# Performance work log

Hardware: AMD Instinct MI355X
Metric: run time of the kernel (lower is better)

The kernel has to match this reference:

```python
import jax, jax.numpy as jnp
import numpy as np

B, S, D = 8, 2048, 512
H, DK, DV = 8, 64, 64


def setup_inputs() -> dict:
    key = jax.random.key(0)
    ks = jax.random.split(key, 12)
    def xavier(k, shape):
        fan_in, fan_out = shape[0], shape[1]
        std = (2.0 / (fan_in + fan_out)) ** 0.5
        return jax.random.normal(k, shape, dtype=jnp.float32) * std
    return {
        "Q": jax.random.normal(ks[0], (B, S, D), dtype=jnp.float32),
        "K": jax.random.normal(ks[1], (B, S, D), dtype=jnp.float32),
        "V": jax.random.normal(ks[2], (B, S, D), dtype=jnp.float32),
        "W_q": xavier(ks[3], (D, H * DK)),
        "W_k": xavier(ks[4], (D, H * DK)),
        "W_v": xavier(ks[5], (D, H * DV)),
        "W_o": xavier(ks[6], (H * DV, D)),
        "W1": xavier(ks[7], (D, D)),  # linear1.weight, stored [out, in]
        "b1": jnp.zeros((D,), dtype=jnp.float32),
        "W2": xavier(ks[8], (D, D)),  # linear2.weight
        "b2": jnp.zeros((D,), dtype=jnp.float32),
    }


def reference(Q, K, V, W_q, W_k, W_v, W_o, W1, b1, W2, b2):
    eps = 1e-6
    bsz, q_len, _ = Q.shape
    # project and split heads: [B, S, H, dk]
    Qh = (Q @ W_q).reshape(bsz, q_len, H, DK)
    Kh = (K @ W_k).reshape(bsz, q_len, H, DK)
    Vh = (V @ W_v).reshape(bsz, q_len, H, DV)
    temperature = DK ** 0.5
    # scores: [B, H, Sq, Sk] (full O(N^2) matrix, as in original)
    scores = jnp.einsum('bqhd,bkhd->bhqk', Qh, Kh) / (temperature + eps)
    probs = jax.nn.softmax(scores, axis=-1)  # dropout = identity (eval)
    V_att = jnp.einsum('bhqk,bkhd->bqhd', probs, Vh).reshape(bsz, q_len, H * DV)
    attn_out = V_att @ W_o  # dropout = identity
    X = Q + attn_out
    # FFN: linear2(relu(linear1(X))); torch Linear: x @ W.T + b
    ffn = jax.nn.relu(X @ W1.T + b1) @ W2.T + b2
    return ffn + X
```

## Files before the change

### kernel.cpp

```cpp
#include <hip/hip_runtime.h>
#include <stdint.h>

typedef __bf16 bf16;
typedef bf16 bf16x8 __attribute__((ext_vector_type(8)));
typedef bf16 bf16x4 __attribute__((ext_vector_type(4)));
typedef float f32x2 __attribute__((ext_vector_type(2)));
typedef float f32x4 __attribute__((ext_vector_type(4)));
typedef float f32x16 __attribute__((ext_vector_type(16)));

#define AS1 __attribute__((address_space(1)))
#define AS3 __attribute__((address_space(3)))

__device__ __forceinline__ void gll16(const void* g, void* l) {
    __builtin_amdgcn_global_load_lds((const AS1 unsigned int*)g,
                                     (AS3 unsigned int*)l, 16, 0, 0);
}

__device__ __forceinline__ bf16 f2bf(float x) { return (bf16)x; }

__device__ __forceinline__ float fexp2(float x) { return __builtin_amdgcn_exp2f(x); }

#define QSCALE_LOG2E 0.18033685757f

__global__ void k_castw(const float* __restrict__ Wq, const float* __restrict__ Wk,
                        const float* __restrict__ Wv, const float* __restrict__ Wo,
                        const float* __restrict__ W1, const float* __restrict__ W2,
                        bf16* __restrict__ oq, bf16* __restrict__ ok, bf16* __restrict__ ov,
                        bf16* __restrict__ oo, bf16* __restrict__ o1, bf16* __restrict__ o2)
{
    const int z = blockIdx.y;
    const int idx = blockIdx.x * 256 + threadIdx.x;
    const float* src = z == 0 ? Wq : z == 1 ? Wk : z == 2 ? Wv : z == 3 ? Wo : z == 4 ? W1 : W2;
    bf16* dst = z == 0 ? oq : z == 1 ? ok : z == 2 ? ov : z == 3 ? oo : z == 4 ? o1 : o2;
    if (z < 4) {
        const int n = idx >> 9, k = idx & 511;
        dst[idx] = f2bf(src[(k << 9) + n]);
    } else {
        dst[idx] = f2bf(src[idx]);
    }
}

__device__ __forceinline__ void gemm_core(const bf16* __restrict__ A,
                                          const bf16* __restrict__ Bt,
                                          const int K, bf16* As, bf16* Bs,
                                          const int bm, const int bn,
                                          f32x4 acc[4][4])
{
    const int tid  = threadIdx.x;
    const int lane = tid & 63;
    const int wave = tid >> 6;
    const int g    = lane >> 4;
    const int l15  = lane & 15;
    const int wm   = (wave >> 1) * 64;
    const int wn   = (wave & 1) * 64;

    const int srow = tid >> 2;
    const int sk   = (tid & 3) * 8;
    const size_t aoff0 = (size_t)(bm + srow) * K + sk;
    const size_t aoff1 = (size_t)(bm + 64 + srow) * K + sk;
    const size_t boff0 = (size_t)(bn + srow) * K + sk;
    const size_t boff1 = (size_t)(bn + 64 + srow) * K + sk;
    char* asb = (char*)As + wave * 1024;
    char* bsb = (char*)Bs + wave * 1024;

    for (int kt = 0; kt < K; kt += 32) {
        __syncthreads();
        gll16(A + aoff0 + kt, asb);
        gll16(A + aoff1 + kt, asb + 4096);
        gll16(Bt + boff0 + kt, bsb);
        gll16(Bt + boff1 + kt, bsb + 4096);
        __syncthreads();
        bf16x8 af[4], bfv[4];
#pragma unroll
        for (int mi = 0; mi < 4; ++mi)
            af[mi] = *(const bf16x8*)&As[(wm + mi * 16 + l15) * 32 + g * 8];
#pragma unroll
        for (int ni = 0; ni < 4; ++ni)
            bfv[ni] = *(const bf16x8*)&Bs[(wn + ni * 16 + l15) * 32 + g * 8];
#pragma unroll
        for (int mi = 0; mi < 4; ++mi)
#pragma unroll
            for (int ni = 0; ni < 4; ++ni)
                acc[mi][ni] = __builtin_amdgcn_mfma_f32_16x16x32_bf16(
                    af[mi], bfv[ni], acc[mi][ni], 0, 0, 0);
    }
}

__device__ __forceinline__ void gemm_core_f32(const float* __restrict__ A,
                                              const bf16* __restrict__ Bt,
                                              const int K, bf16* As, bf16* Bs,
                                              const int bm, const int bn,
                                              f32x4 acc[4][4])
{
    const int tid  = threadIdx.x;
    const int lane = tid & 63;
    const int wave = tid >> 6;
    const int g    = lane >> 4;
    const int l15  = lane & 15;
    const int wm   = (wave >> 1) * 64;
    const int wn   = (wave & 1) * 64;

    const int srow = tid >> 2;
    const int sk   = (tid & 3) * 8;
    const size_t aoff0 = (size_t)(bm + srow) * K + sk;
    const size_t aoff1 = (size_t)(bm + 64 + srow) * K + sk;
    const size_t boff0 = (size_t)(bn + srow) * K + sk;
    const size_t boff1 = (size_t)(bn + 64 + srow) * K + sk;
    char* bsb = (char*)Bs + wave * 1024;
    char* adst = (char*)As + tid * 16;

    for (int kt = 0; kt < K; kt += 32) {
        __syncthreads();
        gll16(Bt + boff0 + kt, bsb);
        gll16(Bt + boff1 + kt, bsb + 4096);
        {
            float4 a0 = *(const float4*)(A + aoff0 + kt);
            float4 a1 = *(const float4*)(A + aoff0 + kt + 4);
            float4 a2 = *(const float4*)(A + aoff1 + kt);
            float4 a3 = *(const float4*)(A + aoff1 + kt + 4);
            bf16x8 c0, c1;
            c0[0] = f2bf(a0.x); c0[1] = f2bf(a0.y); c0[2] = f2bf(a0.z); c0[3] = f2bf(a0.w);
            c0[4] = f2bf(a1.x); c0[5] = f2bf(a1.y); c0[6] = f2bf(a1.z); c0[7] = f2bf(a1.w);
            c1[0] = f2bf(a2.x); c1[1] = f2bf(a2.y); c1[2] = f2bf(a2.z); c1[3] = f2bf(a2.w);
            c1[4] = f2bf(a3.x); c1[5] = f2bf(a3.y); c1[6] = f2bf(a3.z); c1[7] = f2bf(a3.w);
            *(bf16x8*)adst = c0;
            *(bf16x8*)(adst + 4096) = c1;
        }
        __syncthreads();
        bf16x8 af[4], bfv[4];
#pragma unroll
        for (int mi = 0; mi < 4; ++mi)
            af[mi] = *(const bf16x8*)&As[(wm + mi * 16 + l15) * 32 + g * 8];
#pragma unroll
        for (int ni = 0; ni < 4; ++ni)
            bfv[ni] = *(const bf16x8*)&Bs[(wn + ni * 16 + l15) * 32 + g * 8];
#pragma unroll
        for (int mi = 0; mi < 4; ++mi)
#pragma unroll
            for (int ni = 0; ni < 4; ++ni)
                acc[mi][ni] = __builtin_amdgcn_mfma_f32_16x16x32_bf16(
                    af[mi], bfv[ni], acc[mi][ni], 0, 0, 0);
    }
}

template<int EPI>
__global__ __launch_bounds__(256)
void k_gemm(const bf16* __restrict__ A, const bf16* __restrict__ Bt,
            const float* __restrict__ bias, const float* __restrict__ residf,
            const bf16* __restrict__ residb,
            float* __restrict__ Cf, bf16* __restrict__ Cb,
            int M, int N, int K)
{
    __shared__ bf16 As[128 * 32];
    __shared__ bf16 Bs[128 * 32];
    const int bm = blockIdx.y * 128, bn = blockIdx.x * 128;
    f32x4 acc[4][4] = {};
    gemm_core(A, Bt, K, As, Bs, bm, bn, acc);

    const int tid  = threadIdx.x;
    const int lane = tid & 63;
    const int wave = tid >> 6;
    const int g    = lane >> 4;
    const int l15  = lane & 15;
    const int wm   = (wave >> 1) * 64;
    const int wn   = (wave & 1) * 64;
    const int col0 = bn + wn + l15;
#pragma unroll
    for (int ni = 0; ni < 4; ++ni) {
        const int col = col0 + ni * 16;
        float bv = 0.f;
        if constexpr (EPI == 2 || EPI == 3) bv = bias[col];
#pragma unroll
        for (int mi = 0; mi < 4; ++mi) {
#pragma unroll
            for (int r = 0; r < 4; ++r) {
                const int row = bm + wm + mi * 16 + 4 * g + r;
                const size_t idx = (size_t)row * N + col;
                float v = acc[mi][ni][r];
                if constexpr (EPI == 1) {
                    Cb[idx] = f2bf(v + residf[idx]);
                } else if constexpr (EPI == 2) {
                    Cb[idx] = f2bf(fmaxf(v + bv, 0.f));
                } else {
                    Cf[idx] = v + bv + (float)residb[idx];
                }
            }
        }
    }
}

__global__ __launch_bounds__(256)
void k_proj(const float* __restrict__ Qf, const float* __restrict__ Kf, const float* __restrict__ Vf,
            const bf16* __restrict__ BQ, const bf16* __restrict__ BK, const bf16* __restrict__ BV,
            bf16* __restrict__ OQ, bf16* __restrict__ OK_, bf16* __restrict__ OV)
{
    __shared__ bf16 SM[8192];
    const int z = blockIdx.z;
    const float* A = z == 0 ? Qf : z == 1 ? Kf : Vf;
    const bf16* Bt = z == 0 ? BQ : z == 1 ? BK : BV;
    bf16* Cb       = z == 0 ? OQ : z == 1 ? OK_ : OV;
    const int bm = blockIdx.y * 128, bn = blockIdx.x * 128;
    f32x4 acc[4][4] = {};
    gemm_core_f32(A, Bt, 512, SM, SM + 4096, bm, bn, acc);

    const int tid  = threadIdx.x;
    const int lane = tid & 63;
    const int wave = tid >> 6;
    const int g    = lane >> 4;
    const int l15  = lane & 15;
    const int wn   = (wave & 1) * 64;
    const int bb   = bm >> 11;
    const int s0   = bm & 2047;

    __syncthreads();
#pragma unroll
    for (int p = 0; p < 2; ++p) {
        if ((wave >> 1) == p) {
            if (z == 0) {
#pragma unroll
                for (int ni = 0; ni < 4; ++ni) {
                    const int col = wn + ni * 16 + l15;
                    const int hh = col >> 6, dk = col & 63;
                    char* img = (char*)SM + hh * 8192;
#pragma unroll
                    for (int mi = 0; mi < 4; ++mi)
#pragma unroll
                        for (int r = 0; r < 4; ++r) {
                            const int sl = mi * 16 + 4 * g + r;
                            *(bf16*)(img + (sl * 64 + dk) * 2) =
                                f2bf(acc[mi][ni][r] * QSCALE_LOG2E);
                        }
                }
            } else if (z == 1) {
#pragma unroll
                for (int ni = 0; ni < 4; ++ni) {
                    const int col = wn + ni * 16 + l15;
                    const int hh = col >> 6, dk = col & 63;
                    const int ks = dk >> 4, h2 = (dk >> 3) & 1, e = dk & 7;
                    char* img = (char*)SM + hh * 8192;
#pragma unroll
                    for (int mi = 0; mi < 4; ++mi)
#pragma unroll
                        for (int r = 0; r < 4; ++r) {
                            const int sl = mi * 16 + 4 * g + r;
                            const int t2 = sl >> 5, ql = sl & 31;
                            const int off = (((t2 * 4 + ks) * 64 + h2 * 32 + ql) * 8 + e) * 2;
                            *(bf16*)(img + off) = f2bf(acc[mi][ni][r]);
                        }
                }
            } else {
#pragma unroll
                for (int ni = 0; ni < 4; ++ni) {
                    const int col = wn + ni * 16 + l15;
                    const int hh = col >> 6, dv = col & 63;
                    const int dvt = dv >> 5, ql = dv & 31;
                    char* img = (char*)SM + hh * 8192;
#pragma unroll
                    for (int mi = 0; mi < 4; ++mi)
#pragma unroll
                        for (int r = 0; r < 4; ++r) {
                            const int sl = mi * 16 + 4 * g + r;
                            const int kt = sl >> 4, kk = sl & 15;
                            const int h2 = (kk >> 2) & 1;
                            const int e = (kk & 3) | ((kk >> 3) << 2);
                            const int off = (((dvt * 4 + kt) * 64 + h2 * 32 + ql) * 8 + e) * 2;
                            *(bf16*)(img + off) = f2bf(acc[mi][ni][r]);
                        }
                }
            }
        }
        __syncthreads();
        {
            const int hh = tid >> 7, t = tid & 127;
            const int hg = (bn >> 6) + hh;
            const size_t a0 = (size_t)(bb * 8 + hg) * 131072;
            const size_t slab = (z == 0) ? a0 + (size_t)(s0 + p * 64) * 64
                                         : a0 + (size_t)((s0 >> 6) + p) * 4096;
            const char* img = (const char*)SM + hh * 8192;
#pragma unroll
            for (int i = 0; i < 4; ++i) {
                const int G = i * 128 + t;
                bf16x8 vv = *(const bf16x8*)(img + G * 16);
                *(bf16x8*)&Cb[slab + (size_t)G * 8] = vv;
            }
        }
        if (p == 0) __syncthreads();
    }
}

__global__ __launch_bounds__(256, 2)
void k_attn(const bf16* __restrict__ Qp, const bf16* __restrict__ Khp,
            const bf16* __restrict__ Vtp, bf16* __restrict__ O)
{
    __shared__ bf16 smem[16384];
    const int tid = threadIdx.x;
    const int l   = tid & 63;
    const int w   = tid >> 6;
    const int h   = l >> 5;
    const int ql  = l & 31;
    const int d   = blockIdx.x;
    const int bh  = ((d >> 6) << 3) | (d & 7);
    const int qt  = (d >> 3) & 7;
    const size_t base = (size_t)bh * 131072;
    const int q0 = qt * 256 + w * 64;
    const int loff = l * 16;

    bf16x8 qfA[4], qfB[4];
#pragma unroll
    for (int ks = 0; ks < 4; ++ks) {
        qfA[ks] = *(const bf16x8*)&Qp[base + (size_t)(q0 + ql) * 64 + ks * 16 + h * 8];
        qfB[ks] = *(const bf16x8*)&Qp[base + (size_t)(q0 + 32 + ql) * 64 + ks * 16 + h * 8];
    }

    f32x16 oA0 = {}, oA1 = {}, oB0 = {}, oB1 = {};
    float lrunA = 0.f, lrunB = 0.f;

    const bf16* ksrc = Khp + base + tid * 8;
    const bf16* vsrc = Vtp + base + tid * 8;
    char* kb0 = (char*)smem;
    char* kb1 = (char*)smem + 16384;
    const int wdst = w * 1024;

    auto stage = [&](int kvt, char* kb) {
        const bf16* ks = ksrc + kvt * 4096;
        const bf16* vs = vsrc + kvt * 4096;
        gll16(ks,        kb + wdst);
        gll16(ks + 2048, kb + 4096 + wdst);
        gll16(vs,        kb + 8192 + wdst);
        gll16(vs + 2048, kb + 12288 + wdst);
    };

    auto compute = [&](const char* kb) {
        f32x16 sA0 = {}, sA1 = {}, sB0 = {}, sB1 = {};
        __builtin_amdgcn_s_setprio(1);
#pragma unroll
        for (int ks = 0; ks < 4; ++ks) {
            bf16x8 a0 = *(const bf16x8*)(kb + ks * 1024 + loff);
            bf16x8 a1 = *(const bf16x8*)(kb + 4096 + ks * 1024 + loff);
            sA0 = __builtin_amdgcn_mfma_f32_32x32x16_bf16(a0, qfA[ks], sA0, 0, 0, 0);
            sB0 = __builtin_amdgcn_mfma_f32_32x32x16_bf16(a0, qfB[ks], sB0, 0, 0, 0);
            sA1 = __builtin_amdgcn_mfma_f32_32x32x16_bf16(a1, qfA[ks], sA1, 0, 0, 0);
            sB1 = __builtin_amdgcn_mfma_f32_32x32x16_bf16(a1, qfB[ks], sB1, 0, 0, 0);
        }
        __builtin_amdgcn_s_setprio(0);

        f32x2 pA = {0.f, 0.f}, pB = {0.f, 0.f};
#pragma unroll
        for (int r = 0; r < 16; r += 2) {
            sA0[r]     = fexp2(sA0[r]);
            sA0[r + 1] = fexp2(sA0[r + 1]);
            sA1[r]     = fexp2(sA1[r]);
            sA1[r + 1] = fexp2(sA1[r + 1]);
            pA += (f32x2){sA0[r], sA0[r + 1]};
            pA += (f32x2){sA1[r], sA1[r + 1]};
        }
#pragma unroll
        for (int r = 0; r < 16; r += 2) {
            sB0[r]     = fexp2(sB0[r]);
            sB0[r + 1] = fexp2(sB0[r + 1]);
            sB1[r]     = fexp2(sB1[r]);
            sB1[r + 1] = fexp2(sB1[r + 1]);
            pB += (f32x2){sB0[r], sB0[r + 1]};
            pB += (f32x2){sB1[r], sB1[r + 1]};
        }
        lrunA += pA[0] + pA[1];
        lrunB += pB[0] + pB[1];

        bf16x8 pbA[4], pbB[4];
#pragma unroll
        for (int j = 0; j < 4; ++j) {
            const int ofs = 8 * (j & 1);
#pragma unroll
            for (int e = 0; e < 8; ++e) {
                pbA[j][e] = f2bf((j & 2) ? sA1[ofs + e] : sA0[ofs + e]);
                pbB[j][e] = f2bf((j & 2) ? sB1[ofs + e] : sB0[ofs + e]);
            }
        }

        const char* vr = kb + 8192;
        __builtin_amdgcn_s_setprio(1);
#pragma unroll
        for (int j = 0; j < 4; ++j) {
            bf16x8 a0 = *(const bf16x8*)(vr + j * 1024 + loff);
            bf16x8 a1 = *(const bf16x8*)(vr + 4096 + j * 1024 + loff);
            oA0 = __builtin_amdgcn_mfma_f32_32x32x16_bf16(a0, pbA[j], oA0, 0, 0, 0);
            oB0 = __builtin_amdgcn_mfma_f32_32x32x16_bf16(a0, pbB[j], oB0, 0, 0, 0);
            oA1 = __builtin_amdgcn_mfma_f32_32x32x16_bf16(a1, pbA[j], oA1, 0, 0, 0);
            oB1 = __builtin_amdgcn_mfma_f32_32x32x16_bf16(a1, pbB[j], oB1, 0, 0, 0);
        }
        __builtin_amdgcn_s_setprio(0);
    };

    stage(0, kb0);
    __syncthreads();
    for (int kvt = 0; kvt < 32; kvt += 2) {
        if (kvt + 1 < 32) stage(kvt + 1, kb1);
        compute(kb0);
        __syncthreads();
        if (kvt + 2 < 32) stage(kvt + 2, kb0);
        compute(kb1);
        __syncthreads();
    }

    char* ot = (char*)smem + w * 4096;
    const int qr = l >> 1;
    const int dh4 = (l & 1) * 4;
    auto epi = [&](const f32x16& e0, const f32x16& e1, float lr, int qg) {
        lr += __shfl_xor(lr, 32);
        const float inv = 1.f / lr;
#pragma unroll
        for (int dvt = 0; dvt < 2; ++dvt) {
#pragma unroll
            for (int r = 0; r < 16; ++r) {
                const int dv = dvt * 32 + (r & 3) + 8 * (r >> 2) + 4 * h;
                const float val = (dvt ? e1[r] : e0[r]) * inv;
                *(bf16*)(ot + ql * 128 + ((((dv >> 3) ^ (ql & 7)) << 4) | ((dv & 7) << 1))) = f2bf(val);
            }
        }
        const size_t ob = ((size_t)(bh >> 3) * 2048 + qg + qr) * 512 + (bh & 7) * 64 + (size_t)dh4 * 8;
#pragma unroll
        for (int B = 0; B < 4; ++B) {
            bf16x8 v = *(const bf16x8*)(ot + qr * 128 + (((dh4 + B) ^ (qr & 7)) << 4));
            *(bf16x8*)&O[ob + B * 8] = v;
        }
    };
    epi(oA0, oA1, lrunA, q0);
    epi(oB0, oB1, lrunB, q0 + 32);
}

extern "C" void kernel_launch(void* const* d_in, const int* in_sizes, int n_in,
                              void* d_out, int out_size, void* d_ws, size_t ws_size,
                              hipStream_t stream)
{
    const float* Q  = (const float*)d_in[0];
    const float* K  = (const float*)d_in[1];
    const float* V  = (const float*)d_in[2];
    const float* Wq = (const float*)d_in[3];
    const float* Wk = (const float*)d_in[4];
    const float* Wv = (const float*)d_in[5];
    const float* Wo = (const float*)d_in[6];
    const float* W1 = (const float*)d_in[7];
    const float* b1 = (const float*)d_in[8];
    const float* W2 = (const float*)d_in[9];
    const float* b2 = (const float*)d_in[10];
    float* out = (float*)d_out;

    const int M = 8 * 2048;
    const size_t TN = (size_t)M * 512;
    const int WN = 512 * 512;

    char* ws = (char*)d_ws;
    bf16* Qhp  = (bf16*)ws;
    bf16* Khp  = Qhp + TN;
    bf16* Vtp  = Khp + TN;
    bf16* Vatt = Vtp + TN;
    bf16* H1   = Vatt + TN;
    bf16* Xbf  = H1 + TN;
    bf16* Wqt  = Xbf + TN;
    bf16* Wkt  = Wqt + WN;
    bf16* Wvt  = Wkt + WN;
    bf16* Wot  = Wvt + WN;
    bf16* W1b  = Wot + WN;
    bf16* W2b  = W1b + WN;

    k_castw<<<dim3(1024, 6), 256, 0, stream>>>(Wq, Wk, Wv, Wo, W1, W2,
                                               Wqt, Wkt, Wvt, Wot, W1b, W2b);

    k_proj<<<dim3(4, 128, 3), 256, 0, stream>>>(Q, K, V, Wqt, Wkt, Wvt,
                                                Qhp, Khp, Vtp);

    k_attn<<<512, 256, 0, stream>>>(Qhp, Khp, Vtp, Vatt);

    dim3 gg(4, 128);
    k_gemm<1><<<gg, 256, 0, stream>>>(Vatt, Wot, nullptr, Q, nullptr, nullptr, Xbf, M, 512, 512);
    k_gemm<2><<<gg, 256, 0, stream>>>(Xbf, W1b, b1, nullptr, nullptr, nullptr, H1, M, 512, 512);
    k_gemm<3><<<gg, 256, 0, stream>>>(H1, W2b, b2, nullptr, Xbf, out, nullptr, M, 512, 512);
}
```

Measured before the change: 210.2 us.

## Restructure QKV projection to full-width 64-row tiles with register-fed weights

The projection kernel now uses 512-thread blocks that each compute a 64-row by 512-column tile. The fp32 activation tile is converted to bf16 and read from global memory only once per row block instead of four times. Weight fragments are loaded straight from global memory into registers, with no LDS staging, and each of the 8 waves handles one head. The epilogue writes all heads through a single 64KB LDS image. The trade-off is heavier per-wave global weight traffic, and the larger LDS footprint may limit occupancy.

```diff
diff --git a/kernel.cpp b/kernel.cpp
--- a/kernel.cpp
+++ b/kernel.cpp
@@ -69,63 +69,6 @@
         gll16(A + aoff1 + kt, asb + 4096);
         gll16(Bt + boff0 + kt, bsb);
         gll16(Bt + boff1 + kt, bsb + 4096);
-        __syncthreads();
-        bf16x8 af[4], bfv[4];
-#pragma unroll
-        for (int mi = 0; mi < 4; ++mi)
-            af[mi] = *(const bf16x8*)&As[(wm + mi * 16 + l15) * 32 + g * 8];
-#pragma unroll
-        for (int ni = 0; ni < 4; ++ni)
-            bfv[ni] = *(const bf16x8*)&Bs[(wn + ni * 16 + l15) * 32 + g * 8];
-#pragma unroll
-        for (int mi = 0; mi < 4; ++mi)
-#pragma unroll
-            for (int ni = 0; ni < 4; ++ni)
-                acc[mi][ni] = __builtin_amdgcn_mfma_f32_16x16x32_bf16(
-                    af[mi], bfv[ni], acc[mi][ni], 0, 0, 0);
-    }
-}
-
-__device__ __forceinline__ void gemm_core_f32(const float* __restrict__ A,
-                                              const bf16* __restrict__ Bt,
-                                              const int K, bf16* As, bf16* Bs,
-                                              const int bm, const int bn,
-                                              f32x4 acc[4][4])
-{
-    const int tid  = threadIdx.x;
-    const int lane = tid & 63;
-    const int wave = tid >> 6;
-    const int g    = lane >> 4;
-    const int l15  = lane & 15;
-    const int wm   = (wave >> 1) * 64;
-    const int wn   = (wave & 1) * 64;
-
-    const int srow = tid >> 2;
-    const int sk   = (tid & 3) * 8;
-    const size_t aoff0 = (size_t)(bm + srow) * K + sk;
-    const size_t aoff1 = (size_t)(bm + 64 + srow) * K + sk;
-    const size_t boff0 = (size_t)(bn + srow) * K + sk;
-    const size_t boff1 = (size_t)(bn + 64 + srow) * K + sk;
-    char* bsb = (char*)Bs + wave * 1024;
-    char* adst = (char*)As + tid * 16;
-
-    for (int kt = 0; kt < K; kt += 32) {
-        __syncthreads();
-        gll16(Bt + boff0 + kt, bsb);
-        gll16(Bt + boff1 + kt, bsb + 4096);
-        {
-            float4 a0 = *(const float4*)(A + aoff0 + kt);
-            float4 a1 = *(const float4*)(A + aoff0 + kt + 4);
-            float4 a2 = *(const float4*)(A + aoff1 + kt);
-            float4 a3 = *(const float4*)(A + aoff1 + kt + 4);
-            bf16x8 c0, c1;
-            c0[0] = f2bf(a0.x); c0[1] = f2bf(a0.y); c0[2] = f2bf(a0.z); c0[3] = f2bf(a0.w);
-            c0[4] = f2bf(a1.x); c0[5] = f2bf(a1.y); c0[6] = f2bf(a1.z); c0[7] = f2bf(a1.w);
-            c1[0] = f2bf(a2.x); c1[1] = f2bf(a2.y); c1[2] = f2bf(a2.z); c1[3] = f2bf(a2.w);
-            c1[4] = f2bf(a3.x); c1[5] = f2bf(a3.y); c1[6] = f2bf(a3.z); c1[7] = f2bf(a3.w);
-            *(bf16x8*)adst = c0;
-            *(bf16x8*)(adst + 4096) = c1;
-        }
         __syncthreads();
         bf16x8 af[4], bfv[4];
 #pragma unroll
@@ -189,102 +132,113 @@
     }
 }
 
-__global__ __launch_bounds__(256)
+__global__ __launch_bounds__(512, 4)
 void k_proj(const float* __restrict__ Qf, const float* __restrict__ Kf, const float* __restrict__ Vf,
             const bf16* __restrict__ BQ, const bf16* __restrict__ BK, const bf16* __restrict__ BV,
             bf16* __restrict__ OQ, bf16* __restrict__ OK_, bf16* __restrict__ OV)
 {
-    __shared__ bf16 SM[8192];
-    const int z = blockIdx.z;
+    __shared__ char SM[65536];
+    const int z = blockIdx.y;
     const float* A = z == 0 ? Qf : z == 1 ? Kf : Vf;
     const bf16* Bt = z == 0 ? BQ : z == 1 ? BK : BV;
     bf16* Cb       = z == 0 ? OQ : z == 1 ? OK_ : OV;
-    const int bm = blockIdx.y * 128, bn = blockIdx.x * 128;
-    f32x4 acc[4][4] = {};
-    gemm_core_f32(A, Bt, 512, SM, SM + 4096, bm, bn, acc);
-
     const int tid  = threadIdx.x;
     const int lane = tid & 63;
-    const int wave = tid >> 6;
+    const int w    = tid >> 6;
     const int g    = lane >> 4;
     const int l15  = lane & 15;
-    const int wn   = (wave & 1) * 64;
+    const int bm   = blockIdx.x * 64;
     const int bb   = bm >> 11;
     const int s0   = bm & 2047;
 
+    const int arow = tid >> 3, ak0 = (tid & 7) * 4;
+    const size_t abase = (size_t)(bm + arow) * 512 + ak0;
+    const bf16* bbase = Bt + (size_t)(w * 64 + l15) * 512 + g * 8;
+
+    f32x4 acc[4][4] = {};
+
+    for (int kt = 0; kt < 512; kt += 32) {
+        __syncthreads();
+        {
+            float4 a = *(const float4*)(A + abase + kt);
+            bf16x4 c;
+            c[0] = f2bf(a.x); c[1] = f2bf(a.y); c[2] = f2bf(a.z); c[3] = f2bf(a.w);
+            *(bf16x4*)(SM + tid * 8) = c;
+        }
+        bf16x8 bfv[4];
+#pragma unroll
+        for (int ni = 0; ni < 4; ++ni)
+            bfv[ni] = *(const bf16x8*)(bbase + (size_t)ni * 16 * 512 + kt);
+        __syncthreads();
+        bf16x8 af[4];
+#pragma unroll
+        for (int mi = 0; mi < 4; ++mi)
+            af[mi] = *(const bf16x8*)(SM + (mi * 16 + l15) * 64 + g * 16);
+#pragma unroll
+        for (int mi = 0; mi < 4; ++mi)
+#pragma unroll
+            for (int ni = 0; ni < 4; ++ni)
+                acc[mi][ni] = __builtin_amdgcn_mfma_f32_16x16x32_bf16(
+                    af[mi], bfv[ni], acc[mi][ni], 0, 0, 0);
+    }
+
     __syncthreads();
-#pragma unroll
-    for (int p = 0; p < 2; ++p) {
-        if ((wave >> 1) == p) {
-            if (z == 0) {
-#pragma unroll
-                for (int ni = 0; ni < 4; ++ni) {
-                    const int col = wn + ni * 16 + l15;
-                    const int hh = col >> 6, dk = col & 63;
-                    char* img = (char*)SM + hh * 8192;
-#pragma unroll
-                    for (int mi = 0; mi < 4; ++mi)
-#pragma unroll
-                        for (int r = 0; r < 4; ++r) {
-                            const int sl = mi * 16 + 4 * g + r;
-                            *(bf16*)(img + (sl * 64 + dk) * 2) =
-                                f2bf(acc[mi][ni][r] * QSCALE_LOG2E);
-                        }
+    char* img = SM + w * 8192;
+    if (z == 0) {
+#pragma unroll
+        for (int ni = 0; ni < 4; ++ni) {
+            const int dk = ni * 16 + l15;
+#pragma unroll
+            for (int mi = 0; mi < 4; ++mi)
+#pragma unroll
+                for (int r = 0; r < 4; ++r) {
+                    const int sl = mi * 16 + 4 * g + r;
+                    *(bf16*)(img + (sl * 64 + dk) * 2) = f2bf(acc[mi][ni][r] * QSCALE_LOG2E);
                 }
-            } else if (z == 1) {
-#pragma unroll
-                for (int ni = 0; ni < 4; ++ni) {
-                    const int col = wn + ni * 16 + l15;
-                    const int hh = col >> 6, dk = col & 63;
-                    const int ks = dk >> 4, h2 = (dk >> 3) & 1, e = dk & 7;
-                    char* img = (char*)SM + hh * 8192;
-#pragma unroll
-                    for (int mi = 0; mi < 4; ++mi)
-#pragma unroll
-                        for (int r = 0; r < 4; ++r) {
-                            const int sl = mi * 16 + 4 * g + r;
-                            const int t2 = sl >> 5, ql = sl & 31;
-                            const int off = (((t2 * 4 + ks) * 64 + h2 * 32 + ql) * 8 + e) * 2;
-                            *(bf16*)(img + off) = f2bf(acc[mi][ni][r]);
-                        }
+        }
+    } else if (z == 1) {
+#pragma unroll
+        for (int ni = 0; ni < 4; ++ni) {
+            const int dk = ni * 16 + l15;
+            const int ks = dk >> 4, h2 = (dk >> 3) & 1, e = dk & 7;
+#pragma unroll
+            for (int mi = 0; mi < 4; ++mi)
+#pragma unroll
+                for (int r = 0; r < 4; ++r) {
+                    const int sl = mi * 16 + 4 * g + r;
+                    const int t2 = sl >> 5, ql = sl & 31;
+                    *(bf16*)(img + (((t2 * 4 + ks) * 64 + h2 * 32 + ql) * 8 + e) * 2) =
+                        f2bf(acc[mi][ni][r]);
                 }
-            } else {
-#pragma unroll
-                for (int ni = 0; ni < 4; ++ni) {
-                    const int col = wn + ni * 16 + l15;
-                    const int hh = col >> 6, dv = col & 63;
-                    const int dvt = dv >> 5, ql = dv & 31;
-                    char* img = (char*)SM + hh * 8192;
-#pragma unroll
-                    for (int mi = 0; mi < 4; ++mi)
-#pragma unroll
-                        for (int r = 0; r < 4; ++r) {
-                            const int sl = mi * 16 + 4 * g + r;
-                            const int kt = sl >> 4, kk = sl & 15;
-                            const int h2 = (kk >> 2) & 1;
-                            const int e = (kk & 3) | ((kk >> 3) << 2);
-                            const int off = (((dvt * 4 + kt) * 64 + h2 * 32 + ql) * 8 + e) * 2;
-                            *(bf16*)(img + off) = f2bf(acc[mi][ni][r]);
-                        }
+        }
+    } else {
+#pragma unroll
+        for (int ni = 0; ni < 4; ++ni) {
+            const int dk = ni * 16 + l15;
+            const int dvt = dk >> 5, ql = dk & 31;
+#pragma unroll
+            for (int mi = 0; mi < 4; ++mi)
+#pragma unroll
+                for (int r = 0; r < 4; ++r) {
+                    const int sl = mi * 16 + 4 * g + r;
+                    const int ktile = sl >> 4, kk = sl & 15;
+                    const int h2 = (kk >> 2) & 1;
+                    const int e = (kk & 3) | ((kk >> 3) << 2);
+                    *(bf16*)(img + (((dvt * 4 + ktile) * 64 + h2 * 32 + ql) * 8 + e) * 2) =
+                        f2bf(acc[mi][ni][r]);
                 }
-            }
-        }
-        __syncthreads();
-        {
-            const int hh = tid >> 7, t = tid & 127;
-            const int hg = (bn >> 6) + hh;
-            const size_t a0 = (size_t)(bb * 8 + hg) * 131072;
-            const size_t slab = (z == 0) ? a0 + (size_t)(s0 + p * 64) * 64
-                                         : a0 + (size_t)((s0 >> 6) + p) * 4096;
-            const char* img = (const char*)SM + hh * 8192;
-#pragma unroll
-            for (int i = 0; i < 4; ++i) {
-                const int G = i * 128 + t;
-                bf16x8 vv = *(const bf16x8*)(img + G * 16);
-                *(bf16x8*)&Cb[slab + (size_t)G * 8] = vv;
-            }
-        }
-        if (p == 0) __syncthreads();
+        }
+    }
+    __syncthreads();
+#pragma unroll
+    for (int i = 0; i < 8; ++i) {
+        const int G = i * 512 + tid;
+        const int hl = G >> 9;
+        const size_t a0 = (size_t)(bb * 8 + hl) * 131072;
+        const size_t slab = (z == 0) ? a0 + (size_t)s0 * 64
+                                     : a0 + (size_t)(s0 >> 6) * 4096;
+        bf16x8 v = *(const bf16x8*)(SM + G * 16);
+        *(bf16x8*)&Cb[slab + (size_t)(G & 511) * 8] = v;
     }
 }
 
@@ -466,8 +420,8 @@
     k_castw<<<dim3(1024, 6), 256, 0, stream>>>(Wq, Wk, Wv, Wo, W1, W2,
                                                Wqt, Wkt, Wvt, Wot, W1b, W2b);
 
-    k_proj<<<dim3(4, 128, 3), 256, 0, stream>>>(Q, K, V, Wqt, Wkt, Wvt,
-                                                Qhp, Khp, Vtp);
+    k_proj<<<dim3(256, 3), 512, 0, stream>>>(Q, K, V, Wqt, Wkt, Wvt,
+                                             Qhp, Khp, Vtp);
 
     k_attn<<<512, 256, 0, stream>>>(Qhp, Khp, Vtp, Vatt);
 
```

Measured after the change: 206.4 us. About the same (-1.8%).

## Load fp32 activations via direct-to-LDS with swizzle and remap projection blocks for XCD locality

Applied to the files above, without the earlier changes.

The projection kernel now streams fp32 A tiles straight into LDS with global_load_lds using an XOR swizzle, and converts to bf16 when reading LDS fragments. Previously each thread loaded float4 into registers, converted, and stored to LDS. The grid is also flattened to 1D and remapped so blocks sharing the same A rows land on the same XCD, improving L2 reuse across the four N tiles. This raises LDS use to 24KB and moves the conversion into the MFMA inner loop. That may add VALU work per wave, since each wave converts its own fragments redundantly.

```diff
diff --git a/kernel.cpp b/kernel.cpp
--- a/kernel.cpp
+++ b/kernel.cpp
@@ -69,63 +69,6 @@
         gll16(A + aoff1 + kt, asb + 4096);
         gll16(Bt + boff0 + kt, bsb);
         gll16(Bt + boff1 + kt, bsb + 4096);
-        __syncthreads();
-        bf16x8 af[4], bfv[4];
-#pragma unroll
-        for (int mi = 0; mi < 4; ++mi)
-            af[mi] = *(const bf16x8*)&As[(wm + mi * 16 + l15) * 32 + g * 8];
-#pragma unroll
-        for (int ni = 0; ni < 4; ++ni)
-            bfv[ni] = *(const bf16x8*)&Bs[(wn + ni * 16 + l15) * 32 + g * 8];
-#pragma unroll
-        for (int mi = 0; mi < 4; ++mi)
-#pragma unroll
-            for (int ni = 0; ni < 4; ++ni)
-                acc[mi][ni] = __builtin_amdgcn_mfma_f32_16x16x32_bf16(
-                    af[mi], bfv[ni], acc[mi][ni], 0, 0, 0);
-    }
-}
-
-__device__ __forceinline__ void gemm_core_f32(const float* __restrict__ A,
-                                              const bf16* __restrict__ Bt,
-                                              const int K, bf16* As, bf16* Bs,
-                                              const int bm, const int bn,
-                                              f32x4 acc[4][4])
-{
-    const int tid  = threadIdx.x;
-    const int lane = tid & 63;
-    const int wave = tid >> 6;
-    const int g    = lane >> 4;
-    const int l15  = lane & 15;
-    const int wm   = (wave >> 1) * 64;
-    const int wn   = (wave & 1) * 64;
-
-    const int srow = tid >> 2;
-    const int sk   = (tid & 3) * 8;
-    const size_t aoff0 = (size_t)(bm + srow) * K + sk;
-    const size_t aoff1 = (size_t)(bm + 64 + srow) * K + sk;
-    const size_t boff0 = (size_t)(bn + srow) * K + sk;
-    const size_t boff1 = (size_t)(bn + 64 + srow) * K + sk;
-    char* bsb = (char*)Bs + wave * 1024;
-    char* adst = (char*)As + tid * 16;
-
-    for (int kt = 0; kt < K; kt += 32) {
-        __syncthreads();
-        gll16(Bt + boff0 + kt, bsb);
-        gll16(Bt + boff1 + kt, bsb + 4096);
-        {
-            float4 a0 = *(const float4*)(A + aoff0 + kt);
-            float4 a1 = *(const float4*)(A + aoff0 + kt + 4);
-            float4 a2 = *(const float4*)(A + aoff1 + kt);
-            float4 a3 = *(const float4*)(A + aoff1 + kt + 4);
-            bf16x8 c0, c1;
-            c0[0] = f2bf(a0.x); c0[1] = f2bf(a0.y); c0[2] = f2bf(a0.z); c0[3] = f2bf(a0.w);
-            c0[4] = f2bf(a1.x); c0[5] = f2bf(a1.y); c0[6] = f2bf(a1.z); c0[7] = f2bf(a1.w);
-            c1[0] = f2bf(a2.x); c1[1] = f2bf(a2.y); c1[2] = f2bf(a2.z); c1[3] = f2bf(a2.w);
-            c1[4] = f2bf(a3.x); c1[5] = f2bf(a3.y); c1[6] = f2bf(a3.z); c1[7] = f2bf(a3.w);
-            *(bf16x8*)adst = c0;
-            *(bf16x8*)(adst + 4096) = c1;
-        }
         __syncthreads();
         bf16x8 af[4], bfv[4];
 #pragma unroll
@@ -194,24 +137,73 @@
             const bf16* __restrict__ BQ, const bf16* __restrict__ BK, const bf16* __restrict__ BV,
             bf16* __restrict__ OQ, bf16* __restrict__ OK_, bf16* __restrict__ OV)
 {
-    __shared__ bf16 SM[8192];
-    const int z = blockIdx.z;
+    __shared__ char SMRAW[24576];
+    bf16* Bs = (bf16*)(SMRAW + 16384);
+
+    const int dd = blockIdx.x;
+    const int x = dd & 7, q = dd >> 3;
+    const int bnb = q & 3;
+    const int tt = x * 48 + (q >> 2);
+    const int z  = tt >> 7;
+    const int bm = (tt & 127) * 128;
+    const int bn = bnb * 128;
+
     const float* A = z == 0 ? Qf : z == 1 ? Kf : Vf;
     const bf16* Bt = z == 0 ? BQ : z == 1 ? BK : BV;
     bf16* Cb       = z == 0 ? OQ : z == 1 ? OK_ : OV;
-    const int bm = blockIdx.y * 128, bn = blockIdx.x * 128;
-    f32x4 acc[4][4] = {};
-    gemm_core_f32(A, Bt, 512, SM, SM + 4096, bm, bn, acc);
 
     const int tid  = threadIdx.x;
     const int lane = tid & 63;
     const int wave = tid >> 6;
     const int g    = lane >> 4;
     const int l15  = lane & 15;
+    const int wm   = (wave >> 1) * 64;
     const int wn   = (wave & 1) * 64;
-    const int bb   = bm >> 11;
-    const int s0   = bm & 2047;
-
+
+    const int krow = tid >> 3, kc = tid & 7;
+    const size_t aoff = (size_t)(bm + krow) * 512 + ((kc ^ (krow & 7)) << 2);
+    const int srow = tid >> 2;
+    const int sk   = (tid & 3) * 8;
+    const size_t boff0 = (size_t)(bn + srow) * 512 + sk;
+    const size_t boff1 = (size_t)(bn + 64 + srow) * 512 + sk;
+    char* bsb = (char*)Bs + wave * 1024;
+
+    f32x4 acc[4][4] = {};
+
+    for (int kt = 0; kt < 512; kt += 32) {
+        __syncthreads();
+#pragma unroll
+        for (int j = 0; j < 4; ++j)
+            gll16(A + aoff + j * 16384 + kt, SMRAW + j * 4096 + tid * 16);
+        gll16(Bt + boff0 + kt, bsb);
+        gll16(Bt + boff1 + kt, bsb + 4096);
+        __syncthreads();
+        bf16x8 af[4];
+        bf16x8 bfv[4];
+#pragma unroll
+        for (int mi = 0; mi < 4; ++mi) {
+            const int row = wm + mi * 16 + l15;
+            const int r7 = row & 7;
+            float4 lo = *(const float4*)(SMRAW + row * 128 + (((2 * g) ^ r7) << 4));
+            float4 hi = *(const float4*)(SMRAW + row * 128 + (((2 * g + 1) ^ r7) << 4));
+            af[mi][0] = f2bf(lo.x); af[mi][1] = f2bf(lo.y);
+            af[mi][2] = f2bf(lo.z); af[mi][3] = f2bf(lo.w);
+            af[mi][4] = f2bf(hi.x); af[mi][5] = f2bf(hi.y);
+            af[mi][6] = f2bf(hi.z); af[mi][7] = f2bf(hi.w);
+        }
+#pragma unroll
+        for (int ni = 0; ni < 4; ++ni)
+            bfv[ni] = *(const bf16x8*)&Bs[(wn + ni * 16 + l15) * 32 + g * 8];
+#pragma unroll
+        for (int mi = 0; mi < 4; ++mi)
+#pragma unroll
+            for (int ni = 0; ni < 4; ++ni)
+                acc[mi][ni] = __builtin_amdgcn_mfma_f32_16x16x32_bf16(
+                    af[mi], bfv[ni], acc[mi][ni], 0, 0, 0);
+    }
+
+    const int bb = bm >> 11;
+    const int s0 = bm & 2047;
     __syncthreads();
 #pragma unroll
     for (int p = 0; p < 2; ++p) {
@@ -221,7 +213,7 @@
                 for (int ni = 0; ni < 4; ++ni) {
                     const int col = wn + ni * 16 + l15;
                     const int hh = col >> 6, dk = col & 63;
-                    char* img = (char*)SM + hh * 8192;
+                    char* img = SMRAW + hh * 8192;
 #pragma unroll
                     for (int mi = 0; mi < 4; ++mi)
 #pragma unroll
@@ -237,15 +229,15 @@
                     const int col = wn + ni * 16 + l15;
                     const int hh = col >> 6, dk = col & 63;
                     const int ks = dk >> 4, h2 = (dk >> 3) & 1, e = dk & 7;
-                    char* img = (char*)SM + hh * 8192;
+                    char* img = SMRAW + hh * 8192;
 #pragma unroll
                     for (int mi = 0; mi < 4; ++mi)
 #pragma unroll
                         for (int r = 0; r < 4; ++r) {
                             const int sl = mi * 16 + 4 * g + r;
                             const int t2 = sl >> 5, ql = sl & 31;
-                            const int off = (((t2 * 4 + ks) * 64 + h2 * 32 + ql) * 8 + e) * 2;
-                            *(bf16*)(img + off) = f2bf(acc[mi][ni][r]);
+                            *(bf16*)(img + (((t2 * 4 + ks) * 64 + h2 * 32 + ql) * 8 + e) * 2) =
+                                f2bf(acc[mi][ni][r]);
                         }
                 }
             } else {
@@ -254,17 +246,17 @@
                     const int col = wn + ni * 16 + l15;
                     const int hh = col >> 6, dv = col & 63;
                     const int dvt = dv >> 5, ql = dv & 31;
-                    char* img = (char*)SM + hh * 8192;
+                    char* img = SMRAW + hh * 8192;
 #pragma unroll
                     for (int mi = 0; mi < 4; ++mi)
 #pragma unroll
                         for (int r = 0; r < 4; ++r) {
                             const int sl = mi * 16 + 4 * g + r;
-                            const int kt = sl >> 4, kk = sl & 15;
+                            const int ktile = sl >> 4, kk = sl & 15;
                             const int h2 = (kk >> 2) & 1;
                             const int e = (kk & 3) | ((kk >> 3) << 2);
-                            const int off = (((dvt * 4 + kt) * 64 + h2 * 32 + ql) * 8 + e) * 2;
-                            *(bf16*)(img + off) = f2bf(acc[mi][ni][r]);
+                            *(bf16*)(img + (((dvt * 4 + ktile) * 64 + h2 * 32 + ql) * 8 + e) * 2) =
+                                f2bf(acc[mi][ni][r]);
                         }
                 }
             }
@@ -276,7 +268,7 @@
             const size_t a0 = (size_t)(bb * 8 + hg) * 131072;
             const size_t slab = (z == 0) ? a0 + (size_t)(s0 + p * 64) * 64
                                          : a0 + (size_t)((s0 >> 6) + p) * 4096;
-            const char* img = (const char*)SM + hh * 8192;
+            const char* img = SMRAW + hh * 8192;
 #pragma unroll
             for (int i = 0; i < 4; ++i) {
                 const int G = i * 128 + t;
@@ -466,8 +458,8 @@
     k_castw<<<dim3(1024, 6), 256, 0, stream>>>(Wq, Wk, Wv, Wo, W1, W2,
                                                Wqt, Wkt, Wvt, Wot, W1b, W2b);
 
-    k_proj<<<dim3(4, 128, 3), 256, 0, stream>>>(Q, K, V, Wqt, Wkt, Wvt,
-                                                Qhp, Khp, Vtp);
+    k_proj<<<1536, 256, 0, stream>>>(Q, K, V, Wqt, Wkt, Wvt,
+                                     Qhp, Khp, Vtp);
 
     k_attn<<<512, 256, 0, stream>>>(Qhp, Khp, Vtp, Vatt);
 
```

New measurement: 191.7 us (median of 2 runs). -8.8%, faster.
